# Performance work log

Measured on AMD Instinct MI355X. Metric: run time of the kernel, lower is better.

Reference implementation:

```python
import jax, jax.numpy as jnp
import numpy as np

B, D, H, W = 16, 64, 64, 64
K = 1024


def setup_inputs() -> dict:
    key = jax.random.key(0)
    k1, k2 = jax.random.split(key)
    x = jax.random.normal(k1, (B, D, H, W), dtype=jnp.float32)
    limit = 3.0 ** 0.5
    e_i_ts = jax.random.uniform(k2, (D, K), dtype=jnp.float32, minval=-limit, maxval=limit)
    return {"x": x, "e_i_ts": e_i_ts}


def reference(x, e_i_ts):
    b, d, h, w = x.shape
    # [B,H,W,D] -> [N,D]
    flat_x = jnp.transpose(x, (0, 2, 3, 1)).reshape(-1, d)
    distances = (
        jnp.sum(flat_x * flat_x, axis=1, keepdims=True)
        - 2.0 * (flat_x @ e_i_ts)
        + jnp.sum(e_i_ts * e_i_ts, axis=0, keepdims=True)
    )
    encoding_indices = jnp.argmin(distances, axis=1)  # [N]
    reshaped_indices = encoding_indices.reshape(b, h, w)
    # codebook gather: e_i_ts.T is [K,D]
    quantized = jnp.take(e_i_ts.T, reshaped_indices, axis=0)  # [B,H,W,D]
    quantized_x = jnp.transpose(quantized, (0, 3, 1, 2))  # [B,D,H,W]

    dictionary_loss = jnp.mean((jax.lax.stop_gradient(x) - quantized_x) ** 2)
    commitment_loss = jnp.mean((x - jax.lax.stop_gradient(quantized_x)) ** 2)
    # straight-through estimator
    quantized_x = x + jax.lax.stop_gradient(quantized_x - x)
    return quantized_x, dictionary_loss, commitment_loss, encoding_indices.reshape(b, -1)
```

## Files before the change

kernel.cpp:

```cpp
#include <hip/hip_runtime.h>

#define DD 64
#define KK 1024
#define NPTS 65536
#define TOTAL 4194304

#define OFF_L1 4194304
#define OFF_L2 4194305
#define OFF_IDX 4194306

#define WS_ENH_F 64
#define WS_LIST_I 1088
#define RESCUE_CAP 8192
#define WS_EHT_BYTE 65536
#define WS_ELT_BYTE (65536 + 131072)

#define MARGIN_S 0.006f
#define RGRID 512

typedef __attribute__((ext_vector_type(8))) short short8;
typedef __attribute__((ext_vector_type(4))) float f32x4;

__device__ __forceinline__ unsigned short bf16_rne(float f) {
    unsigned b = __float_as_uint(f);
    return (unsigned short)((b + 0x7FFFu + ((b >> 16) & 1u)) >> 16);
}
__device__ __forceinline__ float bf16_to_f(unsigned short h) {
    return __uint_as_float(((unsigned)h) << 16);
}
__device__ __forceinline__ unsigned umax(unsigned a, unsigned b) { return a > b ? a : b; }
__device__ __forceinline__ unsigned umin(unsigned a, unsigned b) { return a < b ? a : b; }
__device__ __forceinline__ void gld_lds16(const void* g, void* l) {
    __builtin_amdgcn_global_load_lds(
        (const __attribute__((address_space(1))) void*)g,
        (__attribute__((address_space(3))) void*)l, 16, 0, 0);
}
__device__ __forceinline__ int swz(int r, int d) {
    return ((d & ~7) ^ ((r & 7) << 3)) | (d & 7);
}

__global__ __launch_bounds__(256) void prep_kernel(const float* __restrict__ e,
                                                   float* __restrict__ enh,
                                                   unsigned short* __restrict__ ehT,
                                                   unsigned short* __restrict__ elT,
                                                   float* __restrict__ sum,
                                                   int* __restrict__ rcnt,
                                                   unsigned* __restrict__ tick) {
    const int tid = threadIdx.x;
    if (blockIdx.x == 0 && tid == 0) { *sum = 0.f; *rcnt = 0; *tick = 0u; }
    const int wave = tid >> 6, lane = tid & 63;
    const int k = blockIdx.x * 4 + wave;
    const float v = e[lane * KK + k];
    const unsigned short h = bf16_rne(v);
    const unsigned short l = bf16_rne(v - bf16_to_f(h));
    const int pos = k * 64 + swz(k, lane);
    ehT[pos] = h;
    elT[pos] = l;
    float s2 = v * v;
#pragma unroll
    for (int m = 32; m > 0; m >>= 1) s2 += __shfl_down(s2, m, 64);
    if (lane == 0) enh[k] = 512.0f - 0.5f * s2;
}

__global__ __launch_bounds__(256) void vq_gemm(const float* __restrict__ x,
                                               const float* __restrict__ e,
                                               const float* __restrict__ enh,
                                               const unsigned short* __restrict__ ehT,
                                               const unsigned short* __restrict__ elT,
                                               float* __restrict__ out,
                                               float* __restrict__ sum,
                                               int* __restrict__ rcnt,
                                               int* __restrict__ rlist) {
    __shared__ __align__(16) char ebuf[2 * 16384];
    __shared__ __align__(16) unsigned short xbh[64 * 64];
    __shared__ __align__(16) unsigned short xbl[64 * 64];
    __shared__ float mv1[64 * 2], mv2[64 * 2];
    __shared__ int mi1[64 * 2];
    __shared__ int ks[64];
    __shared__ float red[4];

    const int tid = threadIdx.x;
    const int wave = tid >> 6, lane = tid & 63;
    const int n0 = blockIdx.x * 64;
    const int b = n0 >> 12;
    const int hw0 = n0 & 4095;

    const char* ehTb = (const char*)ehT;
    const char* elTb = (const char*)elT;
    const int lofs = wave * 1024 + lane * 16;

    {
        char* db = ebuf;
        gld_lds16(ehTb + lofs,        db + wave * 1024);
        gld_lds16(ehTb + 4096 + lofs, db + 4096 + wave * 1024);
        gld_lds16(elTb + lofs,        db + 8192 + wave * 1024);
        gld_lds16(elTb + 4096 + lofs, db + 12288 + wave * 1024);
    }

    float* xsc = (float*)(ebuf + 16384);
    {
        const int d = tid >> 2, ph = tid & 3;
        const float* src = x + ((b * DD + d) << 12) + hw0 + ph * 16;
        float* dst = xsc + d * 64 + ph * 16;
#pragma unroll
        for (int j = 0; j < 4; ++j)
            *(float4*)(dst + j * 4) = *(const float4*)(src + j * 4);
    }
    __syncthreads();
    {
        const int p = tid >> 2, dq = tid & 3;
#pragma unroll
        for (int s = 0; s < 16; ++s) {
            const int d = dq * 16 + s;
            const float f = xsc[d * 64 + p];
            const unsigned short h = bf16_rne(f);
            const int pos = p * 64 + swz(p, d);
            xbh[pos] = h;
            xbl[pos] = bf16_rne(f - bf16_to_f(h));
        }
    }
    __syncthreads();

    const int ln15 = lane & 15, q8 = (lane >> 4) * 8;
    const int wp = (wave >> 1) * 32;
    const int wc = (wave & 1) * 32;

    short8 ah[2][2], al[2][2];
#pragma unroll
    for (int rf = 0; rf < 2; ++rf)
#pragma unroll
        for (int kc = 0; kc < 2; ++kc) {
            const int pp = wp + rf * 16 + ln15;
            const int pos = pp * 64 + ((kc * 32 + q8) ^ ((pp & 7) << 3));
            ah[rf][kc] = *(const short8*)(xbh + pos);
            al[rf][kc] = *(const short8*)(xbl + pos);
        }

    unsigned v1u[8], v2u[8];
#pragma unroll
    for (int r = 0; r < 8; ++r) { v1u[r] = 0u; v2u[r] = 0u; }

    for (int kt = 0; kt < 16; ++kt) {
        __syncthreads();
        if (kt < 15) {
            const int nkt = kt + 1;
            char* db = ebuf + (nkt & 1) * 16384;
            const char* sH = ehTb + nkt * 8192 + lofs;
            const char* sL = elTb + nkt * 8192 + lofs;
            gld_lds16(sH,        db + wave * 1024);
            gld_lds16(sH + 4096, db + 4096 + wave * 1024);
            gld_lds16(sL,        db + 8192 + wave * 1024);
            gld_lds16(sL + 4096, db + 12288 + wave * 1024);
        }
        const unsigned short* ebH = (const unsigned short*)(ebuf + (kt & 1) * 16384);
        const unsigned short* ebL = ebH + 4096;

        f32x4 acc[2][2];
#pragma unroll
        for (int cf = 0; cf < 2; ++cf) {
            const float ec = enh[kt * 64 + wc + cf * 16 + ln15];
#pragma unroll
            for (int rf = 0; rf < 2; ++rf)
                acc[rf][cf] = (f32x4){ec, ec, ec, ec};
        }

#pragma unroll
        for (int kc = 0; kc < 2; ++kc) {
            short8 bh[2], bl[2];
#pragma unroll
            for (int cf = 0; cf < 2; ++cf) {
                const int c = wc + cf * 16 + ln15;
                const int pos = c * 64 + ((kc * 32 + q8) ^ ((c & 7) << 3));
                bh[cf] = *(const short8*)(ebH + pos);
                bl[cf] = *(const short8*)(ebL + pos);
            }
#pragma unroll
            for (int rf = 0; rf < 2; ++rf)
#pragma unroll
                for (int cf = 0; cf < 2; ++cf) {
                    acc[rf][cf] = __builtin_amdgcn_mfma_f32_16x16x32_bf16(al[rf][kc], bh[cf], acc[rf][cf], 0, 0, 0);
                    acc[rf][cf] = __builtin_amdgcn_mfma_f32_16x16x32_bf16(ah[rf][kc], bl[cf], acc[rf][cf], 0, 0, 0);
                    acc[rf][cf] = __builtin_amdgcn_mfma_f32_16x16x32_bf16(ah[rf][kc], bh[cf], acc[rf][cf], 0, 0, 0);
                }
        }

#pragma unroll
        for (int rf = 0; rf < 2; ++rf)
#pragma unroll
            for (int reg = 0; reg < 4; ++reg) {
                const int r = rf * 4 + reg;
                const unsigned k0 = (__float_as_uint(acc[rf][0][reg]) | 31u) ^ (unsigned)(kt * 2 + 0);
                const unsigned k1 = (__float_as_uint(acc[rf][1][reg]) | 31u) ^ (unsigned)(kt * 2 + 1);
                const unsigned a = umax(k0, k1), bb = umin(k0, k1);
                v2u[r] = umax(umax(v2u[r], umin(v1u[r], a)), bb);
                v1u[r] = umax(v1u[r], a);
            }
    }

#pragma unroll
    for (int r = 0; r < 8; ++r) {
        const unsigned c5 = 31u - (v1u[r] & 31u);
        int col = (int)(c5 >> 1) * 64 + wc + (int)(c5 & 1) * 16 + ln15;
        float val = __uint_as_float(v1u[r] & ~31u);
        float sec = __uint_as_float(v2u[r] & ~31u);
#pragma unroll
        for (int msk = 1; msk < 16; msk <<= 1) {
            const float ov = __shfl_xor(val, msk);
            const int oc = __shfl_xor(col, msk);
            const float os = __shfl_xor(sec, msk);
            sec = fmaxf(fmaxf(sec, os), fminf(val, ov));
            const bool t = (ov > val) || (ov == val && oc < col);
            val = t ? ov : val;
            col = t ? oc : col;
        }
        if (ln15 == 0) {
            const int q = lane >> 4;
            const int h = wave & 1;
            const int pt = wp + (r >> 2) * 16 + q * 4 + (r & 3);
            mv1[pt * 2 + h] = val;
            mi1[pt * 2 + h] = col;
            mv2[pt * 2 + h] = sec;
        }
    }
    __syncthreads();
    if (tid < 64) {
        const float va = mv1[tid * 2], vb = mv1[tid * 2 + 1];
        const int ia = mi1[tid * 2], ib = mi1[tid * 2 + 1];
        const bool t = (vb > va) || (vb == va && ib < ia);
        const float bv = t ? vb : va;
        const int bi = t ? ib : ia;
        const float sec = fmaxf(fmaxf(mv2[tid * 2], mv2[tid * 2 + 1]), fminf(va, vb));
        ks[tid] = bi;
        out[OFF_IDX + n0 + tid] = (float)bi;
        if (bv - sec < MARGIN_S) {
            const int w = atomicAdd(rcnt, 1);
            if (w < RESCUE_CAP) rlist[w] = n0 + tid;
        }
    }
    __syncthreads();

    const int p = tid & 63, dqr = tid >> 6;
    const int kp = ks[p];
    float lacc = 0.f;
#pragma unroll
    for (int s = 0; s < 16; ++s) {
        const int d = dqr * 16 + s;
        const float qv = e[d * KK + kp];
        const float xv = x[((b * DD + d) << 12) + hw0 + p];
        out[((b * DD + d) << 12) + hw0 + p] = qv;
        const float df = xv - qv;
        lacc = fmaf(df, df, lacc);
    }
#pragma unroll
    for (int off = 32; off > 0; off >>= 1) lacc += __shfl_down(lacc, off, 64);
    if (lane == 0) red[wave] = lacc;
    __syncthreads();
    if (tid == 0) atomicAdd(sum, red[0] + red[1] + red[2] + red[3]);
}

__global__ __launch_bounds__(256) void rescue_kernel(const float* __restrict__ x,
                                                     const float* __restrict__ e,
                                                     const float* __restrict__ enh,
                                                     const int* __restrict__ rcnt,
                                                     const int* __restrict__ rlist,
                                                     float* __restrict__ out,
                                                     float* __restrict__ sum,
                                                     unsigned* __restrict__ tick) {
    __shared__ float xp[64];
    __shared__ float rv[4];
    __shared__ int ri[4];
    __shared__ int fix[2];
    const int tid = threadIdx.x;
    const int lane = tid & 63, wave = tid >> 6;
    int cnt = *rcnt;
    if (cnt > RESCUE_CAP) cnt = RESCUE_CAP;

    for (int it = blockIdx.x; it < cnt; it += gridDim.x) {
        const int pn = rlist[it];
        const int b = pn >> 12, hw = pn & 4095;
        __syncthreads();
        if (tid < 64) xp[tid] = x[((b * DD + tid) << 12) + hw];
        __syncthreads();
        float dot[4] = {0.f, 0.f, 0.f, 0.f};
#pragma unroll 8
        for (int d = 0; d < DD; ++d) {
            const float xv = xp[d];
            const float4 ev = *(const float4*)(e + d * KK + tid * 4);
            dot[0] = fmaf(xv, ev.x, dot[0]);
            dot[1] = fmaf(xv, ev.y, dot[1]);
            dot[2] = fmaf(xv, ev.z, dot[2]);
            dot[3] = fmaf(xv, ev.w, dot[3]);
        }
        float bv = -3.4e38f;
        int bi = 0;
#pragma unroll
        for (int c = 0; c < 4; ++c) {
            const float a = dot[c] + enh[tid * 4 + c];
            if (a > bv) { bv = a; bi = tid * 4 + c; }
        }
#pragma unroll
        for (int m = 1; m < 64; m <<= 1) {
            const float ov = __shfl_xor(bv, m);
            const int oi = __shfl_xor(bi, m);
            if (ov > bv || (ov == bv && oi < bi)) { bv = ov; bi = oi; }
        }
        if (lane == 0) { rv[wave] = bv; ri[wave] = bi; }
        __syncthreads();
        if (tid == 0) {
            float gb = rv[0];
            int gi = ri[0];
#pragma unroll
            for (int t = 1; t < 4; ++t)
                if (rv[t] > gb || (rv[t] == gb && ri[t] < gi)) { gb = rv[t]; gi = ri[t]; }
            const int kold = (int)out[OFF_IDX + pn];
            fix[0] = (gi != kold) ? gi : -1;
            fix[1] = kold;
        }
        __syncthreads();
        const int kn = fix[0];
        if (kn >= 0 && tid < 64) {
            const int d = tid;
            const float qn = e[d * KK + kn];
            const float qo = e[d * KK + fix[1]];
            const float xv = xp[d];
            out[((b * DD + d) << 12) + hw] = qn;
            float delta = (xv - qn) * (xv - qn) - (xv - qo) * (xv - qo);
#pragma unroll
            for (int off = 32; off > 0; off >>= 1) delta += __shfl_down(delta, off, 64);
            if (tid == 0) {
                atomicAdd(sum, delta);
                out[OFF_IDX + pn] = (float)kn;
            }
        }
    }

    if (tid == 0) {
        __threadfence();
        const unsigned old = atomicAdd(tick, 1u);
        if (old == (unsigned)(gridDim.x - 1)) {
            const float s = atomicAdd(sum, 0.0f);
            const float m = s * (1.0f / (float)TOTAL);
            out[OFF_L1] = m;
            out[OFF_L2] = m;
        }
    }
}

extern "C" void kernel_launch(void* const* d_in, const int* in_sizes, int n_in,
                              void* d_out, int out_size, void* d_ws, size_t ws_size,
                              hipStream_t stream) {
    const float* x = (const float*)d_in[0];
    const float* e = (const float*)d_in[1];
    float* out = (float*)d_out;

    float* sum = (float*)d_ws;
    int* rcnt = (int*)d_ws + 1;
    unsigned* tick = (unsigned*)d_ws + 2;
    float* enh = (float*)d_ws + WS_ENH_F;
    int* rlist = (int*)d_ws + WS_LIST_I;
    unsigned short* ehT = (unsigned short*)((char*)d_ws + WS_EHT_BYTE);
    unsigned short* elT = (unsigned short*)((char*)d_ws + WS_ELT_BYTE);

    prep_kernel<<<256, 256, 0, stream>>>(e, enh, ehT, elT, sum, rcnt, tick);
    vq_gemm<<<NPTS / 64, 256, 0, stream>>>(x, e, enh, ehT, elT, out, sum, rcnt, rlist);
    rescue_kernel<<<RGRID, 256, 0, stream>>>(x, e, enh, rcnt, rlist, out, sum, tick);
}
```

Before: 131.3 us.

## Fuse rescue pass into GEMM kernel and compute loss algebraically

The separate rescue kernel is removed. Near-tie points are now re-checked exactly in fp32 inside each GEMM block, using a per-block list kept in LDS. The loss is computed from ||x||^2 and the best score instead of re-reading x and the codebook. The quantized output is rebuilt from the hi/lo bf16 codebook copies already in the workspace. LDS use is cut by aliasing buffers onto ebuf, with launch bounds set for 5 blocks per CU. The aim is to save a kernel launch and the global rescue traffic, at the cost of serial in-block rescue loops and slight numeric differences in the loss and the gathered values.

```diff
diff --git a/kernel.cpp b/kernel.cpp
--- a/kernel.cpp
+++ b/kernel.cpp
@@ -10,13 +10,10 @@
 #define OFF_IDX 4194306
 
 #define WS_ENH_F 64
-#define WS_LIST_I 1088
-#define RESCUE_CAP 8192
 #define WS_EHT_BYTE 65536
 #define WS_ELT_BYTE (65536 + 131072)
 
 #define MARGIN_S 0.006f
-#define RGRID 512
 
 typedef __attribute__((ext_vector_type(8))) short short8;
 typedef __attribute__((ext_vector_type(4))) float f32x4;
@@ -44,10 +41,9 @@
                                                    unsigned short* __restrict__ ehT,
                                                    unsigned short* __restrict__ elT,
                                                    float* __restrict__ sum,
-                                                   int* __restrict__ rcnt,
                                                    unsigned* __restrict__ tick) {
     const int tid = threadIdx.x;
-    if (blockIdx.x == 0 && tid == 0) { *sum = 0.f; *rcnt = 0; *tick = 0u; }
+    if (blockIdx.x == 0 && tid == 0) { *sum = 0.f; *tick = 0u; }
     const int wave = tid >> 6, lane = tid & 63;
     const int k = blockIdx.x * 4 + wave;
     const float v = e[lane * KK + k];
@@ -62,22 +58,27 @@
     if (lane == 0) enh[k] = 512.0f - 0.5f * s2;
 }
 
-__global__ __launch_bounds__(256) void vq_gemm(const float* __restrict__ x,
-                                               const float* __restrict__ e,
-                                               const float* __restrict__ enh,
-                                               const unsigned short* __restrict__ ehT,
-                                               const unsigned short* __restrict__ elT,
-                                               float* __restrict__ out,
-                                               float* __restrict__ sum,
-                                               int* __restrict__ rcnt,
-                                               int* __restrict__ rlist) {
+__global__ __launch_bounds__(256, 5) void vq_gemm(const float* __restrict__ x,
+                                                  const float* __restrict__ e,
+                                                  const float* __restrict__ enh,
+                                                  const unsigned short* __restrict__ ehT,
+                                                  const unsigned short* __restrict__ elT,
+                                                  float* __restrict__ out,
+                                                  float* __restrict__ sum,
+                                                  unsigned* __restrict__ tick) {
     __shared__ __align__(16) char ebuf[2 * 16384];
-    __shared__ __align__(16) unsigned short xbh[64 * 64];
-    __shared__ __align__(16) unsigned short xbl[64 * 64];
-    __shared__ float mv1[64 * 2], mv2[64 * 2];
-    __shared__ int mi1[64 * 2];
-    __shared__ int ks[64];
-    __shared__ float red[4];
+
+    float* mv1 = (float*)ebuf;
+    float* mv2 = mv1 + 128;
+    int*   mi1 = (int*)(mv2 + 128);
+    int*   ks  = mi1 + 128;
+    float* xnp = (float*)(ks + 64);
+    float* lv  = xnp + 64;
+    float* xp  = lv + 64;
+    int*   rl  = (int*)(xp + 64);
+    int*   rn  = rl + 64;
+    float* rv  = (float*)(rn + 1);
+    int*   ri  = (int*)(rv + 4);
 
     const int tid = threadIdx.x;
     const int wave = tid >> 6, lane = tid & 63;
@@ -107,16 +108,33 @@
             *(float4*)(dst + j * 4) = *(const float4*)(src + j * 4);
     }
     __syncthreads();
+    const int p = tid >> 2, dq = tid & 3;
+    float xv[16];
+    float xn = 0.f;
+#pragma unroll
+    for (int s = 0; s < 16; ++s) {
+        xv[s] = xsc[(dq * 16 + s) * 64 + p];
+        xn = fmaf(xv[s], xv[s], xn);
+    }
+    xn += __shfl_down(xn, 1, 64);
+    xn += __shfl_down(xn, 2, 64);
+    __syncthreads();
+    unsigned short* xbh = (unsigned short*)(ebuf + 16384);
+    unsigned short* xbl = (unsigned short*)(ebuf + 16384 + 8192);
     {
-        const int p = tid >> 2, dq = tid & 3;
-#pragma unroll
-        for (int s = 0; s < 16; ++s) {
-            const int d = dq * 16 + s;
-            const float f = xsc[d * 64 + p];
-            const unsigned short h = bf16_rne(f);
-            const int pos = p * 64 + swz(p, d);
-            xbh[pos] = h;
-            xbl[pos] = bf16_rne(f - bf16_to_f(h));
+#pragma unroll
+        for (int g = 0; g < 2; ++g) {
+            short8 hh, ll;
+#pragma unroll
+            for (int j = 0; j < 8; ++j) {
+                const float f = xv[g * 8 + j];
+                const unsigned short h = bf16_rne(f);
+                hh[j] = (short)h;
+                ll[j] = (short)bf16_rne(f - bf16_to_f(h));
+            }
+            const int pos = p * 64 + ((dq * 16 + g * 8) ^ ((p & 7) << 3));
+            *(short8*)(xbh + pos) = hh;
+            *(short8*)(xbl + pos) = ll;
         }
     }
     __syncthreads();
@@ -197,6 +215,9 @@
             }
     }
 
+    if ((tid & 3) == 0) xnp[p] = xn;
+    if (tid == 0) *rn = 0;
+
 #pragma unroll
     for (int r = 0; r < 8; ++r) {
         const unsigned c5 = 31u - (v1u[r] & 31u);
@@ -231,118 +252,90 @@
         const int bi = t ? ib : ia;
         const float sec = fmaxf(fmaxf(mv2[tid * 2], mv2[tid * 2 + 1]), fminf(va, vb));
         ks[tid] = bi;
-        out[OFF_IDX + n0 + tid] = (float)bi;
+        lv[tid] = xnp[tid] + 1024.0f - 2.0f * bv;
         if (bv - sec < MARGIN_S) {
-            const int w = atomicAdd(rcnt, 1);
-            if (w < RESCUE_CAP) rlist[w] = n0 + tid;
-        }
-    }
-    __syncthreads();
-
-    const int p = tid & 63, dqr = tid >> 6;
-    const int kp = ks[p];
-    float lacc = 0.f;
-#pragma unroll
-    for (int s = 0; s < 16; ++s) {
-        const int d = dqr * 16 + s;
-        const float qv = e[d * KK + kp];
-        const float xv = x[((b * DD + d) << 12) + hw0 + p];
-        out[((b * DD + d) << 12) + hw0 + p] = qv;
-        const float df = xv - qv;
-        lacc = fmaf(df, df, lacc);
-    }
-#pragma unroll
-    for (int off = 32; off > 0; off >>= 1) lacc += __shfl_down(lacc, off, 64);
-    if (lane == 0) red[wave] = lacc;
-    __syncthreads();
-    if (tid == 0) atomicAdd(sum, red[0] + red[1] + red[2] + red[3]);
-}
-
-__global__ __launch_bounds__(256) void rescue_kernel(const float* __restrict__ x,
-                                                     const float* __restrict__ e,
-                                                     const float* __restrict__ enh,
-                                                     const int* __restrict__ rcnt,
-                                                     const int* __restrict__ rlist,
-                                                     float* __restrict__ out,
-                                                     float* __restrict__ sum,
-                                                     unsigned* __restrict__ tick) {
-    __shared__ float xp[64];
-    __shared__ float rv[4];
-    __shared__ int ri[4];
-    __shared__ int fix[2];
-    const int tid = threadIdx.x;
-    const int lane = tid & 63, wave = tid >> 6;
-    int cnt = *rcnt;
-    if (cnt > RESCUE_CAP) cnt = RESCUE_CAP;
-
-    for (int it = blockIdx.x; it < cnt; it += gridDim.x) {
-        const int pn = rlist[it];
-        const int b = pn >> 12, hw = pn & 4095;
+            const int w = atomicAdd(rn, 1);
+            rl[w] = tid;
+        }
+    }
+    __syncthreads();
+
+    const int lcnt = *rn;
+    for (int it = 0; it < lcnt; ++it) {
+        const int pr = rl[it];
+        if (tid < 64) xp[tid] = x[((b * DD + tid) << 12) + hw0 + pr];
         __syncthreads();
-        if (tid < 64) xp[tid] = x[((b * DD + tid) << 12) + hw];
-        __syncthreads();
-        float dot[4] = {0.f, 0.f, 0.f, 0.f};
+        float d0 = 0.f, d1 = 0.f, d2 = 0.f, d3 = 0.f;
 #pragma unroll 8
-        for (int d = 0; d < DD; ++d) {
-            const float xv = xp[d];
-            const float4 ev = *(const float4*)(e + d * KK + tid * 4);
-            dot[0] = fmaf(xv, ev.x, dot[0]);
-            dot[1] = fmaf(xv, ev.y, dot[1]);
-            dot[2] = fmaf(xv, ev.z, dot[2]);
-            dot[3] = fmaf(xv, ev.w, dot[3]);
-        }
-        float bv = -3.4e38f;
-        int bi = 0;
-#pragma unroll
-        for (int c = 0; c < 4; ++c) {
-            const float a = dot[c] + enh[tid * 4 + c];
-            if (a > bv) { bv = a; bi = tid * 4 + c; }
-        }
+        for (int dd = 0; dd < DD; ++dd) {
+            const float xd = xp[dd];
+            const float4 ev = *(const float4*)(e + dd * KK + tid * 4);
+            d0 = fmaf(xd, ev.x, d0);
+            d1 = fmaf(xd, ev.y, d1);
+            d2 = fmaf(xd, ev.z, d2);
+            d3 = fmaf(xd, ev.w, d3);
+        }
+        const float4 ea = *(const float4*)(enh + tid * 4);
+        float bs = d0 + ea.x;
+        int bi2 = tid * 4;
+        if (d1 + ea.y > bs) { bs = d1 + ea.y; bi2 = tid * 4 + 1; }
+        if (d2 + ea.z > bs) { bs = d2 + ea.z; bi2 = tid * 4 + 2; }
+        if (d3 + ea.w > bs) { bs = d3 + ea.w; bi2 = tid * 4 + 3; }
 #pragma unroll
         for (int m = 1; m < 64; m <<= 1) {
-            const float ov = __shfl_xor(bv, m);
-            const int oi = __shfl_xor(bi, m);
-            if (ov > bv || (ov == bv && oi < bi)) { bv = ov; bi = oi; }
-        }
-        if (lane == 0) { rv[wave] = bv; ri[wave] = bi; }
+            const float ov = __shfl_xor(bs, m, 64);
+            const int oi = __shfl_xor(bi2, m, 64);
+            if (ov > bs || (ov == bs && oi < bi2)) { bs = ov; bi2 = oi; }
+        }
+        if (lane == 0) { rv[wave] = bs; ri[wave] = bi2; }
         __syncthreads();
         if (tid == 0) {
-            float gb = rv[0];
+            float gs = rv[0];
             int gi = ri[0];
 #pragma unroll
-            for (int t = 1; t < 4; ++t)
-                if (rv[t] > gb || (rv[t] == gb && ri[t] < gi)) { gb = rv[t]; gi = ri[t]; }
-            const int kold = (int)out[OFF_IDX + pn];
-            fix[0] = (gi != kold) ? gi : -1;
-            fix[1] = kold;
+            for (int t2 = 1; t2 < 4; ++t2)
+                if (rv[t2] > gs || (rv[t2] == gs && ri[t2] < gi)) { gs = rv[t2]; gi = ri[t2]; }
+            ks[pr] = gi;
+            lv[pr] = xnp[pr] + 1024.0f - 2.0f * gs;
         }
         __syncthreads();
-        const int kn = fix[0];
-        if (kn >= 0 && tid < 64) {
-            const int d = tid;
-            const float qn = e[d * KK + kn];
-            const float qo = e[d * KK + fix[1]];
-            const float xv = xp[d];
-            out[((b * DD + d) << 12) + hw] = qn;
-            float delta = (xv - qn) * (xv - qn) - (xv - qo) * (xv - qo);
-#pragma unroll
-            for (int off = 32; off > 0; off >>= 1) delta += __shfl_down(delta, off, 64);
-            if (tid == 0) {
-                atomicAdd(sum, delta);
-                out[OFF_IDX + pn] = (float)kn;
+    }
+
+    if (tid < 64) {
+        out[OFF_IDX + n0 + tid] = (float)ks[tid];
+        float lc = lv[tid];
+#pragma unroll
+        for (int off = 32; off > 0; off >>= 1) lc += __shfl_down(lc, off, 64);
+        if (tid == 0) {
+            atomicAdd(sum, lc);
+            __threadfence();
+            const unsigned old = atomicAdd(tick, 1u);
+            if (old == (unsigned)(gridDim.x - 1)) {
+                const float s = atomicAdd(sum, 0.0f);
+                const float m = s * (1.0f / (float)TOTAL);
+                out[OFF_L1] = m;
+                out[OFF_L2] = m;
             }
         }
     }
 
-    if (tid == 0) {
-        __threadfence();
-        const unsigned old = atomicAdd(tick, 1u);
-        if (old == (unsigned)(gridDim.x - 1)) {
-            const float s = atomicAdd(sum, 0.0f);
-            const float m = s * (1.0f / (float)TOTAL);
-            out[OFF_L1] = m;
-            out[OFF_L2] = m;
-        }
+    {
+        const int pe = tid & 63, dqr = tid >> 6;
+        const int kp = ks[pe];
+        const int kx = (kp & 7) << 3;
+        float qa[16];
+#pragma unroll
+        for (int g = 0; g < 2; ++g) {
+            const int pos = kp * 64 + ((dqr * 16 + g * 8) ^ kx);
+            const short8 h8 = *(const short8*)(ehT + pos);
+            const short8 l8 = *(const short8*)(elT + pos);
+#pragma unroll
+            for (int j = 0; j < 8; ++j)
+                qa[g * 8 + j] = bf16_to_f((unsigned short)h8[j]) + bf16_to_f((unsigned short)l8[j]);
+        }
+        float* ob = out + ((b * DD + dqr * 16) << 12) + hw0 + pe;
+#pragma unroll
+        for (int s = 0; s < 16; ++s) ob[s << 12] = qa[s];
     }
 }
 
@@ -354,14 +347,11 @@
     float* out = (float*)d_out;
 
     float* sum = (float*)d_ws;
-    int* rcnt = (int*)d_ws + 1;
     unsigned* tick = (unsigned*)d_ws + 2;
     float* enh = (float*)d_ws + WS_ENH_F;
-    int* rlist = (int*)d_ws + WS_LIST_I;
     unsigned short* ehT = (unsigned short*)((char*)d_ws + WS_EHT_BYTE);
     unsigned short* elT = (unsigned short*)((char*)d_ws + WS_ELT_BYTE);
 
-    prep_kernel<<<256, 256, 0, stream>>>(e, enh, ehT, elT, sum, rcnt, tick);
-    vq_gemm<<<NPTS / 64, 256, 0, stream>>>(x, e, enh, ehT, elT, out, sum, rcnt, rlist);
-    rescue_kernel<<<RGRID, 256, 0, stream>>>(x, e, enh, rcnt, rlist, out, sum, tick);
-}
+    prep_kernel<<<256, 256, 0, stream>>>(e, enh, ehT, elT, sum, tick);
+    vq_gemm<<<NPTS / 64, 256, 0, stream>>>(x, e, enh, ehT, elT, out, sum, tick);
+}
```

New measurement: 140.6 us. 1.07x slower.
